# Optimization experiments

Hardware: AMD Instinct MI355X
Metric: run time of the kernel (lower is better)

Reference implementation:

```python
import jax, jax.numpy as jnp
import numpy as np

B, N, D, E, G, MID, OUT = 8, 256, 128, 128, 128, 128, 128


def setup_inputs() -> dict:
    key = jax.random.key(0)
    ks = jax.random.split(key, 20)
    s = 0.02
    inp = {
        'node_fts': jax.random.normal(ks[0], (B, N, D), jnp.float32),
        'edge_fts': jax.random.normal(ks[1], (B, N, N, E), jnp.float32),
        'graph_fts': jax.random.normal(ks[2], (B, G), jnp.float32),
        'adj_mat': jax.random.randint(ks[3], (B, N, N), 0, 2, jnp.int32),
        'hidden': jax.random.normal(ks[4], (B, N, D), jnp.float32),
        # message linears (m_n_1, m_h_1, m_e_1, m_g_1)
        'Wn': s * jax.random.normal(ks[5], (D, MID), jnp.float32),
        'bn': jnp.zeros((MID,), jnp.float32),
        'Wh': s * jax.random.normal(ks[6], (D, MID), jnp.float32),
        'bh': jnp.zeros((MID,), jnp.float32),
        'We': s * jax.random.normal(ks[7], (E, MID), jnp.float32),
        'be': jnp.zeros((MID,), jnp.float32),
        'Wg': s * jax.random.normal(ks[8], (G, MID), jnp.float32),
        'bg': jnp.zeros((MID,), jnp.float32),
        # output linears o1 (node), o2 (hidden), o3 (msgs)
        'Wo1': s * jax.random.normal(ks[9], (D, OUT), jnp.float32),
        'bo1': jnp.zeros((OUT,), jnp.float32),
        'Wo2': s * jax.random.normal(ks[10], (D, OUT), jnp.float32),
        'bo2': jnp.zeros((OUT,), jnp.float32),
        'Wo3': s * jax.random.normal(ks[11], (MID, OUT), jnp.float32),
        'bo3': jnp.zeros((OUT,), jnp.float32),
    }
    return inp


def reference(node_fts, edge_fts, graph_fts, adj_mat, hidden,
              Wn, bn, Wh, bh, We, be, Wg, bg,
              Wo1, bo1, Wo2, bo2, Wo3, bo3):
    # Linear projections feeding the broadcast message tensor
    msg_n = node_fts @ Wn + bn          # (B, N, MID)
    msg_h = hidden @ Wh + bh            # (B, N, MID)
    msg_e = edge_fts @ We + be          # (B, N, N, MID)
    msg_g = graph_fts @ Wg + bg         # (B, MID)

    # Broadcast-add into (B, N, N, MID): axis1 <- msg_n (sender), axis2 <- msg_h
    msgs = (msg_n[:, None, :, :] + msg_h[:, :, None, :]
            + msg_e + msg_g[:, None, None, :])

    # Masked max-reduce over axis 1 (msgs_mlp_sizes is None -> no MLP)
    adj = adj_mat.astype(msgs.dtype)[..., None]  # (B, N, N, 1)
    msgs = jnp.max(msgs * adj, axis=1)           # (B, N, MID)

    ret = (node_fts @ Wo1 + bo1) + (hidden @ Wo2 + bo2) + (msgs @ Wo3 + bo3)
    return ret
```

## Files before the change

kernel.cpp:

```cpp
#include <hip/hip_runtime.h>
#include <hip/hip_bf16.h>

#define B_ 8
#define N_ 256
#define C_ 128
#define S_ 8
#define STEPB (N_ * C_ * 4)

typedef __attribute__((ext_vector_type(4))) float f32x4;
typedef __attribute__((ext_vector_type(8))) short s16x8;

typedef __attribute__((address_space(1))) const void gas_void;
typedef __attribute__((address_space(3))) void las_void;

__device__ __forceinline__ unsigned short f2bf(float f) {
  unsigned int u = __builtin_bit_cast(unsigned int, f);
  u += 0x7FFFu + ((u >> 16) & 1u);
  return (unsigned short)(u >> 16);
}

__device__ __forceinline__ unsigned int pk2(float a, float b) {
  __hip_bfloat162 h = __float22bfloat162_rn(make_float2(a, b));
  unsigned int u;
  __builtin_memcpy(&u, &h, 4);
  return u;
}

__device__ __forceinline__ s16x8 cvt8(f32x4 lo, f32x4 hi) {
  union { unsigned int u[4]; s16x8 s; } r;
  r.u[0] = pk2(lo[0], lo[1]);
  r.u[1] = pk2(lo[2], lo[3]);
  r.u[2] = pk2(hi[0], hi[1]);
  r.u[3] = pk2(hi[2], hi[3]);
  return r.s;
}

__global__ void k_pro(const float* __restrict__ node, const float* __restrict__ hidden,
                      const float* __restrict__ graph, const int* __restrict__ adjm,
                      const float* __restrict__ Wn, const float* __restrict__ bn,
                      const float* __restrict__ Wh, const float* __restrict__ bh,
                      const float* __restrict__ be,
                      const float* __restrict__ Wg, const float* __restrict__ bg,
                      const float* __restrict__ We,
                      float* __restrict__ ws_c, unsigned short* __restrict__ ws_mh2,
                      short* __restrict__ ws_B, unsigned char* __restrict__ ws_adj) {
  int bid = blockIdx.x, t = threadIdx.x;
  if (bid >= 544) {
    int base = (bid - 544) * 1024 + t * 8;
    int4 a = *reinterpret_cast<const int4*>(adjm + base);
    int4 c = *reinterpret_cast<const int4*>(adjm + base + 4);
    uint2 v;
    v.x = (unsigned)a.x | ((unsigned)a.y << 8) | ((unsigned)a.z << 16) | ((unsigned)a.w << 24);
    v.y = (unsigned)c.x | ((unsigned)c.y << 8) | ((unsigned)c.z << 16) | ((unsigned)c.w << 24);
    *reinterpret_cast<uint2*>(ws_adj + base) = v;
    return;
  }
  if (bid >= 512) {
    int f = bid - 512;
    if (t < 64) {
      int kb = f >> 3, nbg = f & 7;
      int lr = t & 15, lg = t >> 4;
      s16x8 v;
#pragma unroll
      for (int e = 0; e < 8; ++e)
        v[e] = (short)f2bf(We[(kb * 32 + lg * 8 + e) * C_ + nbg * 16 + lr]);
      *reinterpret_cast<s16x8*>(ws_B + (f * 64 + t) * 8) = v;
    }
    return;
  }
  bool isc = bid < 256;
  int row0 = (isc ? bid : bid - 256) * 8;
  const float* src = isc ? node : hidden;
  const float* W   = isc ? Wn : Wh;
  __shared__ float sh[8][C_];
#pragma unroll
  for (int r = 0; r < 8; ++r) sh[r][t] = src[(row0 + r) * C_ + t];
  __syncthreads();
  float g = 0.f;
  float acc[8];
#pragma unroll
  for (int r = 0; r < 8; ++r) acc[r] = 0.f;
  const float* gr = graph + (row0 >> 8) * C_;
  for (int k = 0; k < C_; k += 8) {
    float wv[8];
#pragma unroll
    for (int u = 0; u < 8; ++u) wv[u] = W[(k + u) * C_ + t];
    if (isc) {
      float wgv[8];
#pragma unroll
      for (int u = 0; u < 8; ++u) wgv[u] = Wg[(k + u) * C_ + t];
#pragma unroll
      for (int u = 0; u < 8; ++u) g += gr[k + u] * wgv[u];
    }
#pragma unroll
    for (int u = 0; u < 8; ++u)
#pragma unroll
      for (int r = 0; r < 8; ++r) acc[r] += sh[r][k + u] * wv[u];
  }
  if (isc) {
    float init = bn[t] + be[t] + bg[t] + g;
#pragma unroll
    for (int r = 0; r < 8; ++r) ws_c[(row0 + r) * C_ + t] = acc[r] + init;
  } else {
    float init = bh[t];
    int p = (t >> 5) * 32 + (t & 15) * 2 + ((t >> 4) & 1);
#pragma unroll
    for (int r = 0; r < 8; ++r) ws_mh2[(row0 + r) * C_ + p] = f2bf(acc[r] + init);
  }
}

__global__ __launch_bounds__(256, 4) void k_main(
    const float* __restrict__ edge, const unsigned char* __restrict__ ws_adj,
    const short* __restrict__ ws_B,
    const float* __restrict__ ws_c, const unsigned short* __restrict__ ws_mh2,
    float* __restrict__ pbuf) {
  __shared__ __align__(16) char smem[3 * 8192 + 8192 + 512];
  char* ring    = smem;
  char* mh_lds  = smem + 24576;
  char* adj_lds = smem + 24576 + 8192;
  const int lane = threadIdx.x & 63;
  const int w = threadIdx.x >> 6;
  const int wg = blockIdx.x;
  const int s   = wg & 7;
  const int j16 = (wg >> 3) & 15;
  const int b   = wg >> 7;
  const int j0 = j16 * 16;
  const int n0 = w * 32;
  const int i0 = s * 32;
  const int lr = lane & 15;
  const int lg = lane >> 4;

  s16x8 bfrag[4][2];
#pragma unroll
  for (int kb = 0; kb < 4; ++kb)
#pragma unroll
    for (int nb = 0; nb < 2; ++nb)
      bfrag[kb][nb] = *reinterpret_cast<const s16x8*>(
          ws_B + ((kb * 8 + w * 2 + nb) * 64 + lane) * 8);

  float cf[2][4];
#pragma unroll
  for (int nb = 0; nb < 2; ++nb)
#pragma unroll
    for (int r = 0; r < 4; ++r)
      cf[nb][r] = ws_c[(b * N_ + j0 + lg * 4 + r) * C_ + n0 + nb * 16 + lr];

  f32x4 mx[2];
#pragma unroll
  for (int nb = 0; nb < 2; ++nb)
#pragma unroll
    for (int r = 0; r < 4; ++r) mx[nb][r] = -INFINITY;

  const char* gedge = (const char*)(edge + ((size_t)(b * N_ + i0) * N_ + j0) * C_);

  int soff[2];
#pragma unroll
  for (int q = 0; q < 2; ++q) {
    int y = w * 2048 + q * 1024 + lane * 16;
    int row = y >> 9;
    soff[q] = y ^ ((row & 7) << 4);
  }
  const int base0 = lr * 512 + lg * 32;
  const int swz = (lr & 7) << 4;

#define GLL16(GP, LP) __builtin_amdgcn_global_load_lds((gas_void*)(GP), (las_void*)(LP), 16, 0, 0)
#define GLL4(GP, LP)  __builtin_amdgcn_global_load_lds((gas_void*)(GP), (las_void*)(LP), 4, 0, 0)

#define ISSUE(SL, TT) do { \
    const char* gch = gedge + (size_t)(TT) * STEPB; \
    char* lb = ring + (SL) * 8192 + w * 2048; \
    GLL16(gch + soff[0], lb); \
    GLL16(gch + soff[1], lb + 1024); \
  } while (0)

  {
    const char* mh_g = (const char*)(ws_mh2 + ((size_t)(b * N_) + i0) * C_);
    GLL16(mh_g + w * 2048 + lane * 16, mh_lds + w * 2048);
    GLL16(mh_g + w * 2048 + 1024 + lane * 16, mh_lds + w * 2048 + 1024);
    const char* adj_g = (const char*)(ws_adj + ((size_t)(b * N_) + i0) * N_ + j0);
    GLL4(adj_g + (lane >> 2) * N_ + (lane & 3) * 4, adj_lds);
    GLL4(adj_g + ((lane >> 2) + 16) * N_ + (lane & 3) * 4, adj_lds + 256);
  }
  ISSUE(0, 0);
  ISSUE(1, 1);
  asm volatile("s_waitcnt vmcnt(4)\n\ts_barrier" ::: "memory");

#define STEP(SL, ISL, WAITN, DOISSUE, TI, T) do { \
    asm volatile("s_waitcnt vmcnt(" WAITN ")\n\ts_barrier" ::: "memory"); \
    if (DOISSUE) ISSUE(ISL, TI); \
    const char* rb = ring + (SL) * 8192; \
    s16x8 af[4]; \
    _Pragma("unroll") \
    for (int kb = 0; kb < 4; ++kb) { \
      int a0 = (base0 + kb * 128) ^ swz; \
      f32x4 lo = *reinterpret_cast<const f32x4*>(rb + a0); \
      f32x4 hi = *reinterpret_cast<const f32x4*>(rb + (a0 ^ 16)); \
      af[kb] = cvt8(lo, hi); \
    } \
    unsigned int mw = *reinterpret_cast<const unsigned int*>(mh_lds + (T) * 256 + w * 64 + lr * 4); \
    unsigned int ab = *reinterpret_cast<const unsigned int*>(adj_lds + (T) * 16 + lg * 4); \
    float mh0 = __builtin_bit_cast(float, mw << 16); \
    float mh1 = __builtin_bit_cast(float, mw & 0xffff0000u); \
    float adjf[4] = {(float)(ab & 0xff), (float)((ab >> 8) & 0xff), \
                     (float)((ab >> 16) & 0xff), (float)(ab >> 24)}; \
    _Pragma("unroll") \
    for (int nb = 0; nb < 2; ++nb) { \
      f32x4 acc; \
      float mhv = nb ? mh1 : mh0; \
      _Pragma("unroll") \
      for (int r = 0; r < 4; ++r) acc[r] = cf[nb][r] + mhv; \
      _Pragma("unroll") \
      for (int kb = 0; kb < 4; ++kb) \
        acc = __builtin_amdgcn_mfma_f32_16x16x32_bf16(af[kb], bfrag[kb][nb], acc, 0, 0, 0); \
      _Pragma("unroll") \
      for (int r = 0; r < 4; ++r) mx[nb][r] = fmaxf(mx[nb][r], adjf[r] * acc[r]); \
    } \
  } while (0)

  for (int o = 0; o < 10; ++o) {
    STEP(0, 2, "2", 1, 3 * o + 2, 3 * o);
    STEP(1, 0, "2", 1, 3 * o + 3, 3 * o + 1);
    STEP(2, 1, "2", 1, 3 * o + 4, 3 * o + 2);
  }
  STEP(0, 2, "2", 0, 0, 30);
  STEP(1, 0, "0", 0, 0, 31);

#undef STEP
#undef ISSUE
#undef GLL16
#undef GLL4

  float* prow = pbuf + (((size_t)s * B_ + b) * N_ + j0 + lg * 4) * C_ + n0 + lr;
#pragma unroll
  for (int nb = 0; nb < 2; ++nb)
#pragma unroll
    for (int r = 0; r < 4; ++r)
      prow[r * C_ + nb * 16] = mx[nb][r];
}

__global__ void k_epi(const float* __restrict__ node, const float* __restrict__ hidden,
                      const float* __restrict__ Wo1, const float* __restrict__ bo1,
                      const float* __restrict__ Wo2, const float* __restrict__ bo2,
                      const float* __restrict__ Wo3, const float* __restrict__ bo3,
                      const float* __restrict__ pbuf, float* __restrict__ out) {
  int row0 = blockIdx.x * 4;
  int col = threadIdx.x & 127;
  int half = threadIdx.x >> 7;
  __shared__ float shn[4][C_], shh[4][C_], shm[4][C_];
#pragma unroll
  for (int r = 0; r < 2; ++r) {
    int rr = half * 2 + r;
    shn[rr][col] = node[(row0 + rr) * C_ + col];
    shh[rr][col] = hidden[(row0 + rr) * C_ + col];
    float mv = -INFINITY;
#pragma unroll
    for (int s = 0; s < S_; ++s)
      mv = fmaxf(mv, pbuf[((size_t)s * (B_ * N_) + row0 + rr) * C_ + col]);
    shm[rr][col] = mv;
  }
  __syncthreads();
  float init = bo1[col] + bo2[col] + bo3[col];
  float acc[2];
  acc[0] = init; acc[1] = init;
  for (int k = 0; k < C_; k += 8) {
    float wv1[8], wv2[8], wv3[8];
#pragma unroll
    for (int u = 0; u < 8; ++u) {
      wv1[u] = Wo1[(k + u) * C_ + col];
      wv2[u] = Wo2[(k + u) * C_ + col];
      wv3[u] = Wo3[(k + u) * C_ + col];
    }
#pragma unroll
    for (int u = 0; u < 8; ++u)
#pragma unroll
      for (int r = 0; r < 2; ++r) {
        int rr = half * 2 + r;
        acc[r] += shn[rr][k + u] * wv1[u] + shh[rr][k + u] * wv2[u] + shm[rr][k + u] * wv3[u];
      }
  }
#pragma unroll
  for (int r = 0; r < 2; ++r)
    out[(row0 + half * 2 + r) * C_ + col] = acc[r];
}

extern "C" void kernel_launch(void* const* d_in, const int* in_sizes, int n_in,
                              void* d_out, int out_size, void* d_ws, size_t ws_size,
                              hipStream_t stream) {
  const float* node   = (const float*)d_in[0];
  const float* edge   = (const float*)d_in[1];
  const float* graph  = (const float*)d_in[2];
  const int*   adjm   = (const int*)d_in[3];
  const float* hidden = (const float*)d_in[4];
  const float* Wn = (const float*)d_in[5];  const float* bn = (const float*)d_in[6];
  const float* Wh = (const float*)d_in[7];  const float* bh = (const float*)d_in[8];
  const float* We = (const float*)d_in[9];  const float* be = (const float*)d_in[10];
  const float* Wg = (const float*)d_in[11]; const float* bg = (const float*)d_in[12];
  const float* Wo1 = (const float*)d_in[13]; const float* bo1 = (const float*)d_in[14];
  const float* Wo2 = (const float*)d_in[15]; const float* bo2 = (const float*)d_in[16];
  const float* Wo3 = (const float*)d_in[17]; const float* bo3 = (const float*)d_in[18];
  float* out = (float*)d_out;

  char* ws = (char*)d_ws;
  float*          ws_c   = (float*)ws;
  unsigned short* ws_mh2 = (unsigned short*)(ws + (1u << 20));
  short*          ws_B   = (short*)(ws + 1572864u);
  unsigned char*  ws_adj = (unsigned char*)(ws + 1835008u);
  float*          pbuf   = (float*)(ws + (4u << 20));

  k_pro<<<1056, 128, 0, stream>>>(node, hidden, graph, adjm, Wn, bn, Wh, bh, be,
                                  Wg, bg, We, ws_c, ws_mh2, ws_B, ws_adj);
  k_main<<<1024, 256, 0, stream>>>(edge, ws_adj, ws_B, ws_c, ws_mh2, pbuf);
  k_epi<<<512, 256, 0, stream>>>(node, hidden, Wo1, bo1, Wo2, bo2, Wo3, bo3,
                                 pbuf, out);
}
```

Baseline: 88.14 us.

## Interleave i-rows across split blocks, deepen edge ring, split-K prologue and epilogue

```diff
diff --git a/kernel.cpp b/kernel.cpp
--- a/kernel.cpp
+++ b/kernel.cpp
@@ -6,6 +6,7 @@
 #define C_ 128
 #define S_ 8
 #define STEPB (N_ * C_ * 4)
+#define SLOT 8704
 
 typedef __attribute__((ext_vector_type(4))) float f32x4;
 typedef __attribute__((ext_vector_type(8))) short s16x8;
@@ -45,8 +46,8 @@
                       float* __restrict__ ws_c, unsigned short* __restrict__ ws_mh2,
                       short* __restrict__ ws_B, unsigned char* __restrict__ ws_adj) {
   int bid = blockIdx.x, t = threadIdx.x;
-  if (bid >= 544) {
-    int base = (bid - 544) * 1024 + t * 8;
+  if (bid >= 1032) {
+    int base = (bid - 1032) * 2048 + t * 8;
     int4 a = *reinterpret_cast<const int4*>(adjm + base);
     int4 c = *reinterpret_cast<const int4*>(adjm + base + 4);
     uint2 v;
@@ -55,57 +56,70 @@
     *reinterpret_cast<uint2*>(ws_adj + base) = v;
     return;
   }
-  if (bid >= 512) {
-    int f = bid - 512;
-    if (t < 64) {
-      int kb = f >> 3, nbg = f & 7;
-      int lr = t & 15, lg = t >> 4;
-      s16x8 v;
-#pragma unroll
-      for (int e = 0; e < 8; ++e)
-        v[e] = (short)f2bf(We[(kb * 32 + lg * 8 + e) * C_ + nbg * 16 + lr]);
-      *reinterpret_cast<s16x8*>(ws_B + (f * 64 + t) * 8) = v;
-    }
+  if (bid >= 1024) {
+    int f = (bid - 1024) * 4 + (t >> 6);
+    int tl = t & 63;
+    int kb = f >> 3, nbg = f & 7;
+    int lr = tl & 15, lg = tl >> 4;
+    s16x8 v;
+#pragma unroll
+    for (int e = 0; e < 8; ++e)
+      v[e] = (short)f2bf(We[(kb * 32 + lg * 8 + e) * C_ + nbg * 16 + lr]);
+    *reinterpret_cast<s16x8*>(ws_B + (f * 64 + tl) * 8) = v;
     return;
   }
-  bool isc = bid < 256;
-  int row0 = (isc ? bid : bid - 256) * 8;
+  bool isc = bid < 512;
+  int row0 = (isc ? bid : bid - 512) * 4;
+  int col = t & 127, kh = t >> 7;
   const float* src = isc ? node : hidden;
   const float* W   = isc ? Wn : Wh;
-  __shared__ float sh[8][C_];
-#pragma unroll
-  for (int r = 0; r < 8; ++r) sh[r][t] = src[(row0 + r) * C_ + t];
+  __shared__ float sh[4][C_];
+  __shared__ float shp[5][C_];
+  {
+    int i0 = t, i1 = t + 256;
+    sh[i0 >> 7][i0 & 127] = src[(row0 + (i0 >> 7)) * C_ + (i0 & 127)];
+    sh[i1 >> 7][i1 & 127] = src[(row0 + (i1 >> 7)) * C_ + (i1 & 127)];
+  }
   __syncthreads();
   float g = 0.f;
-  float acc[8];
-#pragma unroll
-  for (int r = 0; r < 8; ++r) acc[r] = 0.f;
+  float acc[4] = {0.f, 0.f, 0.f, 0.f};
   const float* gr = graph + (row0 >> 8) * C_;
-  for (int k = 0; k < C_; k += 8) {
+  int kbase = kh * 64;
+  for (int k = 0; k < 64; k += 8) {
     float wv[8];
 #pragma unroll
-    for (int u = 0; u < 8; ++u) wv[u] = W[(k + u) * C_ + t];
+    for (int u = 0; u < 8; ++u) wv[u] = W[(kbase + k + u) * C_ + col];
     if (isc) {
       float wgv[8];
 #pragma unroll
-      for (int u = 0; u < 8; ++u) wgv[u] = Wg[(k + u) * C_ + t];
-#pragma unroll
-      for (int u = 0; u < 8; ++u) g += gr[k + u] * wgv[u];
+      for (int u = 0; u < 8; ++u) wgv[u] = Wg[(kbase + k + u) * C_ + col];
+#pragma unroll
+      for (int u = 0; u < 8; ++u) g += gr[kbase + k + u] * wgv[u];
     }
 #pragma unroll
     for (int u = 0; u < 8; ++u)
 #pragma unroll
-      for (int r = 0; r < 8; ++r) acc[r] += sh[r][k + u] * wv[u];
-  }
-  if (isc) {
-    float init = bn[t] + be[t] + bg[t] + g;
-#pragma unroll
-    for (int r = 0; r < 8; ++r) ws_c[(row0 + r) * C_ + t] = acc[r] + init;
-  } else {
-    float init = bh[t];
-    int p = (t >> 5) * 32 + (t & 15) * 2 + ((t >> 4) & 1);
-#pragma unroll
-    for (int r = 0; r < 8; ++r) ws_mh2[(row0 + r) * C_ + p] = f2bf(acc[r] + init);
+      for (int r = 0; r < 4; ++r) acc[r] += sh[r][kbase + k + u] * wv[u];
+  }
+  if (kh) {
+#pragma unroll
+    for (int r = 0; r < 4; ++r) shp[r][col] = acc[r];
+    shp[4][col] = g;
+  }
+  __syncthreads();
+  if (!kh) {
+#pragma unroll
+    for (int r = 0; r < 4; ++r) acc[r] += shp[r][col];
+    g += shp[4][col];
+    if (isc) {
+      float init = bn[col] + be[col] + bg[col] + g;
+#pragma unroll
+      for (int r = 0; r < 4; ++r) ws_c[(row0 + r) * C_ + col] = acc[r] + init;
+    } else {
+      int p = (col >> 5) * 32 + (col & 15) * 2 + ((col >> 4) & 1);
+#pragma unroll
+      for (int r = 0; r < 4; ++r) ws_mh2[(row0 + r) * C_ + p] = f2bf(acc[r] + bh[col]);
+    }
   }
 }
 
@@ -114,19 +128,15 @@
     const short* __restrict__ ws_B,
     const float* __restrict__ ws_c, const unsigned short* __restrict__ ws_mh2,
     float* __restrict__ pbuf) {
-  __shared__ __align__(16) char smem[3 * 8192 + 8192 + 512];
-  char* ring    = smem;
-  char* mh_lds  = smem + 24576;
-  char* adj_lds = smem + 24576 + 8192;
+  __shared__ __align__(16) char smem[4 * SLOT];
   const int lane = threadIdx.x & 63;
   const int w = threadIdx.x >> 6;
   const int wg = blockIdx.x;
-  const int s   = wg & 7;
+  const int b   = wg & 7;
   const int j16 = (wg >> 3) & 15;
-  const int b   = wg >> 7;
+  const int s   = wg >> 7;
   const int j0 = j16 * 16;
   const int n0 = w * 32;
-  const int i0 = s * 32;
   const int lr = lane & 15;
   const int lg = lane >> 4;
 
@@ -151,7 +161,9 @@
 #pragma unroll
     for (int r = 0; r < 4; ++r) mx[nb][r] = -INFINITY;
 
-  const char* gedge = (const char*)(edge + ((size_t)(b * N_ + i0) * N_ + j0) * C_);
+  const char* gedge = (const char*)(edge + ((size_t)(b * N_ + s) * N_ + j0) * C_);
+  const char* gmh   = (const char*)ws_mh2 + (size_t)(b * N_ + s) * 256;
+  const char* gadj  = (const char*)(ws_adj + (size_t)b * N_ * N_ + (size_t)s * N_);
 
   int soff[2];
 #pragma unroll
@@ -167,28 +179,18 @@
 #define GLL4(GP, LP)  __builtin_amdgcn_global_load_lds((gas_void*)(GP), (las_void*)(LP), 4, 0, 0)
 
 #define ISSUE(SL, TT) do { \
-    const char* gch = gedge + (size_t)(TT) * STEPB; \
-    char* lb = ring + (SL) * 8192 + w * 2048; \
-    GLL16(gch + soff[0], lb); \
-    GLL16(gch + soff[1], lb + 1024); \
+    char* lb = smem + (SL) * SLOT; \
+    const char* gch = gedge + (size_t)(TT) * 8 * STEPB; \
+    GLL16(gch + soff[0], lb + w * 2048); \
+    GLL16(gch + soff[1], lb + w * 2048 + 1024); \
+    GLL4(gmh + (size_t)(TT) * 8 * 256 + lane * 4, lb + 8192); \
+    GLL4(gadj + (size_t)(TT) * 8 * N_ + lane * 4, lb + 8448); \
   } while (0)
 
-  {
-    const char* mh_g = (const char*)(ws_mh2 + ((size_t)(b * N_) + i0) * C_);
-    GLL16(mh_g + w * 2048 + lane * 16, mh_lds + w * 2048);
-    GLL16(mh_g + w * 2048 + 1024 + lane * 16, mh_lds + w * 2048 + 1024);
-    const char* adj_g = (const char*)(ws_adj + ((size_t)(b * N_) + i0) * N_ + j0);
-    GLL4(adj_g + (lane >> 2) * N_ + (lane & 3) * 4, adj_lds);
-    GLL4(adj_g + ((lane >> 2) + 16) * N_ + (lane & 3) * 4, adj_lds + 256);
-  }
-  ISSUE(0, 0);
-  ISSUE(1, 1);
-  asm volatile("s_waitcnt vmcnt(4)\n\ts_barrier" ::: "memory");
-
-#define STEP(SL, ISL, WAITN, DOISSUE, TI, T) do { \
+#define STEP(SL, ISL, WAITN, DOISSUE, TI) do { \
     asm volatile("s_waitcnt vmcnt(" WAITN ")\n\ts_barrier" ::: "memory"); \
     if (DOISSUE) ISSUE(ISL, TI); \
-    const char* rb = ring + (SL) * 8192; \
+    const char* rb = smem + (SL) * SLOT; \
     s16x8 af[4]; \
     _Pragma("unroll") \
     for (int kb = 0; kb < 4; ++kb) { \
@@ -197,8 +199,8 @@
       f32x4 hi = *reinterpret_cast<const f32x4*>(rb + (a0 ^ 16)); \
       af[kb] = cvt8(lo, hi); \
     } \
-    unsigned int mw = *reinterpret_cast<const unsigned int*>(mh_lds + (T) * 256 + w * 64 + lr * 4); \
-    unsigned int ab = *reinterpret_cast<const unsigned int*>(adj_lds + (T) * 16 + lg * 4); \
+    unsigned int mw = *reinterpret_cast<const unsigned int*>(rb + 8192 + w * 64 + lr * 4); \
+    unsigned int ab = *reinterpret_cast<const unsigned int*>(rb + 8448 + j0 + lg * 4); \
     float mh0 = __builtin_bit_cast(float, mw << 16); \
     float mh1 = __builtin_bit_cast(float, mw & 0xffff0000u); \
     float adjf[4] = {(float)(ab & 0xff), (float)((ab >> 8) & 0xff), \
@@ -217,13 +219,20 @@
     } \
   } while (0)
 
-  for (int o = 0; o < 10; ++o) {
-    STEP(0, 2, "2", 1, 3 * o + 2, 3 * o);
-    STEP(1, 0, "2", 1, 3 * o + 3, 3 * o + 1);
-    STEP(2, 1, "2", 1, 3 * o + 4, 3 * o + 2);
-  }
-  STEP(0, 2, "2", 0, 0, 30);
-  STEP(1, 0, "0", 0, 0, 31);
+  ISSUE(0, 0);
+  ISSUE(1, 1);
+  ISSUE(2, 2);
+
+  for (int o = 0; o < 7; ++o) {
+    STEP(0, 3, "8", 1, 4 * o + 3);
+    STEP(1, 0, "8", 1, 4 * o + 4);
+    STEP(2, 1, "8", 1, 4 * o + 5);
+    STEP(3, 2, "8", 1, 4 * o + 6);
+  }
+  STEP(0, 3, "8", 1, 31);
+  STEP(1, 0, "8", 0, 0);
+  STEP(2, 1, "4", 0, 0);
+  STEP(3, 2, "0", 0, 0);
 
 #undef STEP
 #undef ISSUE
@@ -243,44 +252,46 @@
                       const float* __restrict__ Wo2, const float* __restrict__ bo2,
                       const float* __restrict__ Wo3, const float* __restrict__ bo3,
                       const float* __restrict__ pbuf, float* __restrict__ out) {
-  int row0 = blockIdx.x * 4;
-  int col = threadIdx.x & 127;
-  int half = threadIdx.x >> 7;
-  __shared__ float shn[4][C_], shh[4][C_], shm[4][C_];
-#pragma unroll
-  for (int r = 0; r < 2; ++r) {
-    int rr = half * 2 + r;
-    shn[rr][col] = node[(row0 + rr) * C_ + col];
-    shh[rr][col] = hidden[(row0 + rr) * C_ + col];
+  int row0 = blockIdx.x * 2;
+  int t = threadIdx.x;
+  int col = t & 127, kh = t >> 7;
+  __shared__ float shn[2][C_], shh[2][C_], shm[2][C_], shp[2][C_];
+  {
+    int r = t >> 7, c = t & 127;
+    shn[r][c] = node[(row0 + r) * C_ + c];
+    shh[r][c] = hidden[(row0 + r) * C_ + c];
     float mv = -INFINITY;
 #pragma unroll
     for (int s = 0; s < S_; ++s)
-      mv = fmaxf(mv, pbuf[((size_t)s * (B_ * N_) + row0 + rr) * C_ + col]);
-    shm[rr][col] = mv;
+      mv = fmaxf(mv, pbuf[((size_t)s * (B_ * N_) + row0 + r) * C_ + c]);
+    shm[r][c] = mv;
   }
   __syncthreads();
-  float init = bo1[col] + bo2[col] + bo3[col];
-  float acc[2];
-  acc[0] = init; acc[1] = init;
-  for (int k = 0; k < C_; k += 8) {
+  float acc[2] = {0.f, 0.f};
+  int kbase = kh * 64;
+  for (int k = 0; k < 64; k += 8) {
     float wv1[8], wv2[8], wv3[8];
 #pragma unroll
     for (int u = 0; u < 8; ++u) {
-      wv1[u] = Wo1[(k + u) * C_ + col];
-      wv2[u] = Wo2[(k + u) * C_ + col];
-      wv3[u] = Wo3[(k + u) * C_ + col];
+      wv1[u] = Wo1[(kbase + k + u) * C_ + col];
+      wv2[u] = Wo2[(kbase + k + u) * C_ + col];
+      wv3[u] = Wo3[(kbase + k + u) * C_ + col];
     }
 #pragma unroll
     for (int u = 0; u < 8; ++u)
 #pragma unroll
-      for (int r = 0; r < 2; ++r) {
-        int rr = half * 2 + r;
-        acc[r] += shn[rr][k + u] * wv1[u] + shh[rr][k + u] * wv2[u] + shm[rr][k + u] * wv3[u];
-      }
-  }
-#pragma unroll
-  for (int r = 0; r < 2; ++r)
-    out[(row0 + half * 2 + r) * C_ + col] = acc[r];
+      for (int r = 0; r < 2; ++r)
+        acc[r] += shn[r][kbase + k + u] * wv1[u] + shh[r][kbase + k + u] * wv2[u]
+                + shm[r][kbase + k + u] * wv3[u];
+  }
+  if (kh) { shp[0][col] = acc[0]; shp[1][col] = acc[1]; }
+  __syncthreads();
+  if (!kh) {
+    float init = bo1[col] + bo2[col] + bo3[col];
+#pragma unroll
+    for (int r = 0; r < 2; ++r)
+      out[(row0 + r) * C_ + col] = acc[r] + shp[r][col] + init;
+  }
 }
 
 extern "C" void kernel_launch(void* const* d_in, const int* in_sizes, int n_in,
@@ -307,9 +318,9 @@
   unsigned char*  ws_adj = (unsigned char*)(ws + 1835008u);
   float*          pbuf   = (float*)(ws + (4u << 20));
 
-  k_pro<<<1056, 128, 0, stream>>>(node, hidden, graph, adjm, Wn, bn, Wh, bh, be,
+  k_pro<<<1288, 256, 0, stream>>>(node, hidden, graph, adjm, Wn, bn, Wh, bh, be,
                                   Wg, bg, We, ws_c, ws_mh2, ws_B, ws_adj);
   k_main<<<1024, 256, 0, stream>>>(edge, ws_adj, ws_B, ws_c, ws_mh2, pbuf);
-  k_epi<<<512, 256, 0, stream>>>(node, hidden, Wo1, bo1, Wo2, bo2, Wo3, bo3,
-                                 pbuf, out);
-}
+  k_epi<<<1024, 256, 0, stream>>>(node, hidden, Wo1, bo1, Wo2, bo2, Wo3, bo3,
+                                  pbuf, out);
+}
```

Measured after the change: 223.5 us. 2.54x slower.

## Interleave sender rows across splits, deepen ring to four slots, store partials in bf16

Applied to the files above, without the earlier changes.

```diff
diff --git a/kernel.cpp b/kernel.cpp
--- a/kernel.cpp
+++ b/kernel.cpp
@@ -6,6 +6,7 @@
 #define C_ 128
 #define S_ 8
 #define STEPB (N_ * C_ * 4)
+#define SLOT 8704
 
 typedef __attribute__((ext_vector_type(4))) float f32x4;
 typedef __attribute__((ext_vector_type(8))) short s16x8;
@@ -113,20 +114,16 @@
     const float* __restrict__ edge, const unsigned char* __restrict__ ws_adj,
     const short* __restrict__ ws_B,
     const float* __restrict__ ws_c, const unsigned short* __restrict__ ws_mh2,
-    float* __restrict__ pbuf) {
-  __shared__ __align__(16) char smem[3 * 8192 + 8192 + 512];
-  char* ring    = smem;
-  char* mh_lds  = smem + 24576;
-  char* adj_lds = smem + 24576 + 8192;
+    unsigned short* __restrict__ pbuf) {
+  __shared__ __align__(16) char smem[4 * SLOT];
   const int lane = threadIdx.x & 63;
   const int w = threadIdx.x >> 6;
   const int wg = blockIdx.x;
-  const int s   = wg & 7;
+  const int b   = wg & 7;
   const int j16 = (wg >> 3) & 15;
-  const int b   = wg >> 7;
+  const int s   = wg >> 7;
   const int j0 = j16 * 16;
   const int n0 = w * 32;
-  const int i0 = s * 32;
   const int lr = lane & 15;
   const int lg = lane >> 4;
 
@@ -151,7 +148,9 @@
 #pragma unroll
     for (int r = 0; r < 4; ++r) mx[nb][r] = -INFINITY;
 
-  const char* gedge = (const char*)(edge + ((size_t)(b * N_ + i0) * N_ + j0) * C_);
+  const char* gedge = (const char*)(edge + ((size_t)(b * N_ + s) * N_ + j0) * C_);
+  const char* gmh   = (const char*)ws_mh2 + (size_t)(b * N_ + s) * 256;
+  const char* gadj  = (const char*)(ws_adj + (size_t)b * N_ * N_ + (size_t)s * N_);
 
   int soff[2];
 #pragma unroll
@@ -167,28 +166,18 @@
 #define GLL4(GP, LP)  __builtin_amdgcn_global_load_lds((gas_void*)(GP), (las_void*)(LP), 4, 0, 0)
 
 #define ISSUE(SL, TT) do { \
-    const char* gch = gedge + (size_t)(TT) * STEPB; \
-    char* lb = ring + (SL) * 8192 + w * 2048; \
-    GLL16(gch + soff[0], lb); \
-    GLL16(gch + soff[1], lb + 1024); \
+    char* lb = smem + (SL) * SLOT; \
+    const char* gch = gedge + (size_t)(TT) * 8 * STEPB; \
+    GLL16(gch + soff[0], lb + w * 2048); \
+    GLL16(gch + soff[1], lb + w * 2048 + 1024); \
+    GLL4(gmh + (size_t)(TT) * 8 * 256 + lane * 4, lb + 8192); \
+    GLL4(gadj + (size_t)(TT) * 8 * N_ + lane * 4, lb + 8448); \
   } while (0)
 
-  {
-    const char* mh_g = (const char*)(ws_mh2 + ((size_t)(b * N_) + i0) * C_);
-    GLL16(mh_g + w * 2048 + lane * 16, mh_lds + w * 2048);
-    GLL16(mh_g + w * 2048 + 1024 + lane * 16, mh_lds + w * 2048 + 1024);
-    const char* adj_g = (const char*)(ws_adj + ((size_t)(b * N_) + i0) * N_ + j0);
-    GLL4(adj_g + (lane >> 2) * N_ + (lane & 3) * 4, adj_lds);
-    GLL4(adj_g + ((lane >> 2) + 16) * N_ + (lane & 3) * 4, adj_lds + 256);
-  }
-  ISSUE(0, 0);
-  ISSUE(1, 1);
-  asm volatile("s_waitcnt vmcnt(4)\n\ts_barrier" ::: "memory");
-
-#define STEP(SL, ISL, WAITN, DOISSUE, TI, T) do { \
+#define STEP(SL, ISL, WAITN, DOISSUE, TI) do { \
     asm volatile("s_waitcnt vmcnt(" WAITN ")\n\ts_barrier" ::: "memory"); \
     if (DOISSUE) ISSUE(ISL, TI); \
-    const char* rb = ring + (SL) * 8192; \
+    const char* rb = smem + (SL) * SLOT; \
     s16x8 af[4]; \
     _Pragma("unroll") \
     for (int kb = 0; kb < 4; ++kb) { \
@@ -197,8 +186,8 @@
       f32x4 hi = *reinterpret_cast<const f32x4*>(rb + (a0 ^ 16)); \
       af[kb] = cvt8(lo, hi); \
     } \
-    unsigned int mw = *reinterpret_cast<const unsigned int*>(mh_lds + (T) * 256 + w * 64 + lr * 4); \
-    unsigned int ab = *reinterpret_cast<const unsigned int*>(adj_lds + (T) * 16 + lg * 4); \
+    unsigned int mw = *reinterpret_cast<const unsigned int*>(rb + 8192 + w * 64 + lr * 4); \
+    unsigned int ab = *reinterpret_cast<const unsigned int*>(rb + 8448 + j0 + lg * 4); \
     float mh0 = __builtin_bit_cast(float, mw << 16); \
     float mh1 = __builtin_bit_cast(float, mw & 0xffff0000u); \
     float adjf[4] = {(float)(ab & 0xff), (float)((ab >> 8) & 0xff), \
@@ -217,32 +206,39 @@
     } \
   } while (0)
 
-  for (int o = 0; o < 10; ++o) {
-    STEP(0, 2, "2", 1, 3 * o + 2, 3 * o);
-    STEP(1, 0, "2", 1, 3 * o + 3, 3 * o + 1);
-    STEP(2, 1, "2", 1, 3 * o + 4, 3 * o + 2);
-  }
-  STEP(0, 2, "2", 0, 0, 30);
-  STEP(1, 0, "0", 0, 0, 31);
+  ISSUE(0, 0);
+  ISSUE(1, 1);
+  ISSUE(2, 2);
+
+  for (int o = 0; o < 7; ++o) {
+    STEP(0, 3, "8", 1, 4 * o + 3);
+    STEP(1, 0, "8", 1, 4 * o + 4);
+    STEP(2, 1, "8", 1, 4 * o + 5);
+    STEP(3, 2, "8", 1, 4 * o + 6);
+  }
+  STEP(0, 3, "8", 1, 31);
+  STEP(1, 0, "8", 0, 0);
+  STEP(2, 1, "4", 0, 0);
+  STEP(3, 2, "0", 0, 0);
 
 #undef STEP
 #undef ISSUE
 #undef GLL16
 #undef GLL4
 
-  float* prow = pbuf + (((size_t)s * B_ + b) * N_ + j0 + lg * 4) * C_ + n0 + lr;
+  unsigned short* prow = pbuf + (((size_t)s * B_ + b) * N_ + j0 + lg * 4) * C_ + n0 + lr;
 #pragma unroll
   for (int nb = 0; nb < 2; ++nb)
 #pragma unroll
     for (int r = 0; r < 4; ++r)
-      prow[r * C_ + nb * 16] = mx[nb][r];
+      prow[r * C_ + nb * 16] = f2bf(mx[nb][r]);
 }
 
 __global__ void k_epi(const float* __restrict__ node, const float* __restrict__ hidden,
                       const float* __restrict__ Wo1, const float* __restrict__ bo1,
                       const float* __restrict__ Wo2, const float* __restrict__ bo2,
                       const float* __restrict__ Wo3, const float* __restrict__ bo3,
-                      const float* __restrict__ pbuf, float* __restrict__ out) {
+                      const unsigned short* __restrict__ pbuf, float* __restrict__ out) {
   int row0 = blockIdx.x * 4;
   int col = threadIdx.x & 127;
   int half = threadIdx.x >> 7;
@@ -254,8 +250,10 @@
     shh[rr][col] = hidden[(row0 + rr) * C_ + col];
     float mv = -INFINITY;
 #pragma unroll
-    for (int s = 0; s < S_; ++s)
-      mv = fmaxf(mv, pbuf[((size_t)s * (B_ * N_) + row0 + rr) * C_ + col]);
+    for (int s = 0; s < S_; ++s) {
+      unsigned int u = pbuf[((size_t)s * (B_ * N_) + row0 + rr) * C_ + col];
+      mv = fmaxf(mv, __builtin_bit_cast(float, u << 16));
+    }
     shm[rr][col] = mv;
   }
   __syncthreads();
@@ -305,7 +303,7 @@
   unsigned short* ws_mh2 = (unsigned short*)(ws + (1u << 20));
   short*          ws_B   = (short*)(ws + 1572864u);
   unsigned char*  ws_adj = (unsigned char*)(ws + 1835008u);
-  float*          pbuf   = (float*)(ws + (4u << 20));
+  unsigned short* pbuf   = (unsigned short*)(ws + (4u << 20));
 
   k_pro<<<1056, 128, 0, stream>>>(node, hidden, graph, adjm, Wn, bn, Wh, bh, be,
                                   Wg, bg, We, ws_c, ws_mh2, ws_B, ws_adj);
```

Result: faster. 85.27 us (-3.3%).
